# Kernel tuning notes

Hardware: AMD Instinct MI355X
Metric: run time of the kernel (lower is better)

The kernel has to match this reference:

```python
import jax, jax.numpy as jnp
import numpy as np

# dims
B, N, D = 4, 1024, 768
H, HD = 12, 64            # num_heads, head_dim (routed q heads = top-H experts)
EA = 24                   # num_attn_experts
EF, KF = 8, 2             # num_ffd_experts, ffd_heads (top-k for FFN MoE)
HS = int(4 * D) // KF     # ffn expert head_size = 1536
T = 9                     # task_num
S = 1                     # shared FFN experts: max(1, int(8*0.1))


def layernorm(x, g, b, eps=1e-5):
    m = x.mean(-1, keepdims=True)
    v = ((x - m) ** 2).mean(-1, keepdims=True)
    return (x - m) * jax.lax.rsqrt(v + eps) * g + b


def setup_inputs() -> dict:
    key = jax.random.key(0)
    ks = jax.random.split(key, 16)
    s = 0.02
    rn = lambda k, shp: jax.random.normal(k, shp, dtype=jnp.float32)
    return {
        "x": rn(ks[0], (B, N, D)),
        "task_bh": 3,
        "ln1_g": jnp.ones((D,), jnp.float32), "ln1_b": jnp.zeros((D,), jnp.float32),
        "ln2_g": jnp.ones((D,), jnp.float32), "ln2_b": jnp.zeros((D,), jnp.float32),
        "gate_a": rn(ks[1], (T, D, EA)) * s,
        "Wq_in": rn(ks[2], (EA, D, HD)) * s,
        "Wq_out": rn(ks[3], (EA, HD, D)) * s,
        "W_kv": rn(ks[4], (D, 2 * HD)) * s, "b_kv": jnp.zeros((2 * HD,), jnp.float32),
        "gate_f": rn(ks[5], (T, D, EF)) * s,
        "W1f": rn(ks[6], (EF, D, HS)) * s, "b1f": jnp.zeros((EF, HS), jnp.float32),
        "W2f": rn(ks[7], (EF, HS, D)) * s, "b_out": jnp.zeros((D,), jnp.float32),
        "Ws1": rn(ks[8], (S, D, HS)) * s, "bs1": jnp.zeros((S, HS), jnp.float32),
        "Ws2": rn(ks[9], (S, HS, D)) * s,
    }


def _route(h, gate_w, k):
    # h: [B,N,D], gate_w: [D,E] -> normalized top-k weights + one-hot dispatch
    probs = jax.nn.softmax(jnp.einsum("bnd,de->bne", h, gate_w), axis=-1)
    topv, topi = jax.lax.top_k(probs, k)                 # [B,N,k]
    topv = topv / topv.sum(-1, keepdims=True)
    oh = jax.nn.one_hot(topi, probs.shape[-1], dtype=h.dtype)  # [B,N,k,E]
    return topv, oh


def reference(x, task_bh, ln1_g, ln1_b, ln2_g, ln2_b, gate_a, Wq_in, Wq_out,
              W_kv, b_kv, gate_f, W1f, b1f, W2f, b_out, Ws1, bs1, Ws2):
    # --- MoE attention (routed q heads, shared single-head k/v) ---
    h = layernorm(x, ln1_g, ln1_b)
    topv, oh = _route(h, gate_a[task_bh], H)             # [B,N,H], [B,N,H,EA]
    h_all = jnp.einsum("bnd,edh->bneh", h, Wq_in)        # all-expert q projections
    q = jnp.einsum("bnke,bneh->bnkh", oh, h_all)         # gathered q heads [B,N,H,HD]
    kv = h @ W_kv + b_kv
    kk, vv = kv[..., :HD], kv[..., HD:]                  # [B,N,HD]
    att = jnp.einsum("bihd,bjd->bhij", q, kk) * (HD ** -0.5)
    att = jax.nn.softmax(att, axis=-1)
    o = jnp.einsum("bhij,bjd->bihd", att, vv)            # [B,N,H,HD]
    dense = jnp.einsum("bnk,bnke,bnkh->bneh", topv, oh, o)  # scatter to experts
    y = jnp.einsum("bneh,ehd->bnd", dense, Wq_out)       # gated expert output proj
    x = x + y

    # --- MoE FFN (top-KF routed experts + shared experts) ---
    h = layernorm(x, ln2_g, ln2_b)
    topv, oh = _route(h, gate_f[task_bh], KF)            # [B,N,KF], [B,N,KF,EF]
    h_all = jax.nn.gelu(jnp.einsum("bnd,edh->bneh", h, W1f) + b1f, approximate=False)
    wdense = jnp.einsum("bnk,bnke->bne", topv, oh)       # per-expert gate weights
    y = jnp.einsum("bne,bneh,ehd->bnd", wdense, h_all, W2f) + b_out
    hs = jax.nn.gelu(jnp.einsum("bnd,sdh->bnsh", h, Ws1) + bs1, approximate=False)
    y = y + jnp.einsum("bnsh,shd->bnd", hs, Ws2)         # always-on shared experts
    return x + y
```

## Files before the change

### kernel.cpp

```cpp
#include <hip/hip_runtime.h>
#include <hip/hip_bf16.h>

#define NTOK 4096
#define DDIM 768
#define NEA  24
#define NHEAD 12
#define HDIM 64
#define NEF  8
#define HSD  1536
#define SEQL 1024
#define NB   4
#define MAXTILE 104

using bf16 = __hip_bfloat16;

typedef float v4f __attribute__((ext_vector_type(4)));
typedef short v8s __attribute__((ext_vector_type(8)));
typedef __bf16 v8bf __attribute__((ext_vector_type(8)));

typedef __attribute__((address_space(3))) unsigned lds_u32_t;
typedef const __attribute__((address_space(1))) unsigned glb_u32_t;

__device__ __forceinline__ void gload16(const void* g, void* l) {
  __builtin_amdgcn_global_load_lds((glb_u32_t*)g, (lds_u32_t*)l, 16, 0, 0);
}

__device__ __forceinline__ float gelu_f(float x) {
  return 0.5f * x * (1.0f + erff(x * 0.70710678118654752440f));
}

__device__ __forceinline__ short f2bf_s(float x) {
  bf16 h = __float2bfloat16(x);
  return __builtin_bit_cast(short, h);
}

__device__ __forceinline__ void gemm_core(const short* gA0, const short* gA1,
                                          const short* gB0, const short* gB1,
                                          short* lA, short* lB, int steps,
                                          v4f (&acc)[4][4])
{
  const int tid = threadIdx.x;
  const int w = tid >> 6, l = tid & 63;
  const int wr = (w >> 1) * 64, wc = (w & 1) * 64;
  const int fr = l & 15, ko = (l >> 4) * 8;
  const int sb = w * 1024;
  gload16(gA0, lA + sb); gload16(gA1, lA + sb + 512);
  gload16(gB0, lB + sb); gload16(gB1, lB + sb + 512);
  gA0 += 32; gA1 += 32; gB0 += 32; gB1 += 32;
  __syncthreads();
  int cur = 0;
  for (int s = 0; s < steps; ++s) {
    const int nxt = cur ^ 1;
    if (s + 1 < steps) {
      gload16(gA0, lA + nxt * 4096 + sb);
      gload16(gA1, lA + nxt * 4096 + sb + 512);
      gload16(gB0, lB + nxt * 4096 + sb);
      gload16(gB1, lB + nxt * 4096 + sb + 512);
      gA0 += 32; gA1 += 32; gB0 += 32; gB1 += 32;
    }
    const short* bA = lA + cur * 4096;
    const short* bB = lB + cur * 4096;
    v8s av[4], bv[4];
#pragma unroll
    for (int mi = 0; mi < 4; ++mi)
      av[mi] = *(const v8s*)(bA + (wr + mi * 16 + fr) * 32 + ko);
#pragma unroll
    for (int ni = 0; ni < 4; ++ni)
      bv[ni] = *(const v8s*)(bB + (wc + ni * 16 + fr) * 32 + ko);
#pragma unroll
    for (int mi = 0; mi < 4; ++mi)
#pragma unroll
      for (int ni = 0; ni < 4; ++ni)
        acc[mi][ni] = __builtin_amdgcn_mfma_f32_16x16x32_bf16(
            __builtin_bit_cast(v8bf, av[mi]), __builtin_bit_cast(v8bf, bv[ni]),
            acc[mi][ni], 0, 0, 0);
    __syncthreads();
    cur = nxt;
  }
}

template<int EPI>
__global__ __launch_bounds__(256, 4) void k_gemm(const short* __restrict__ A,
    const short* __restrict__ Bt, float* __restrict__ C,
    const float* __restrict__ bias, const float* __restrict__ addsrc,
    int N, int K)
{
  __shared__ __align__(16) short lA[2 * 128 * 32];
  __shared__ __align__(16) short lB[2 * 128 * 32];
  const int tid = threadIdx.x, w = tid >> 6, l = tid & 63;
  const int m0 = blockIdx.x * 128, n0 = blockIdx.y * 128;
  const int ca = w * 128 + l, cb = ca + 64;
  const short* gA0 = A + (size_t)(m0 + (ca >> 2)) * K + (ca & 3) * 8;
  const short* gA1 = A + (size_t)(m0 + (cb >> 2)) * K + (cb & 3) * 8;
  const short* gB0 = Bt + (size_t)(n0 + (ca >> 2)) * K + (ca & 3) * 8;
  const short* gB1 = Bt + (size_t)(n0 + (cb >> 2)) * K + (cb & 3) * 8;
  v4f acc[4][4];
  v4f z = {0.f, 0.f, 0.f, 0.f};
#pragma unroll
  for (int i = 0; i < 4; ++i)
#pragma unroll
    for (int j = 0; j < 4; ++j) acc[i][j] = z;
  gemm_core(gA0, gA1, gB0, gB1, lA, lB, K >> 5, acc);
  const int wr = (w >> 1) * 64, wc = (w & 1) * 64;
  const int fr = l & 15, rq = (l >> 4) * 4;
#pragma unroll
  for (int mi = 0; mi < 4; ++mi)
#pragma unroll
    for (int ni = 0; ni < 4; ++ni)
#pragma unroll
      for (int j = 0; j < 4; ++j) {
        int rg = m0 + wr + mi * 16 + rq + j;
        int cg = n0 + wc + ni * 16 + fr;
        float v = acc[mi][ni][j];
        if (EPI == 1) v += bias[cg];
        if (EPI == 2) v += addsrc[(size_t)rg * N + cg];
        C[(size_t)rg * N + cg] = v;
      }
}

template<int PHASE>
__global__ __launch_bounds__(256, 4) void k_gemm_moe(
    const short* __restrict__ Aact, const short* __restrict__ Wt,
    const short* __restrict__ Wst, const float* __restrict__ b1f,
    const float* __restrict__ bs1, const float* __restrict__ wsl,
    const int* __restrict__ off, const int* __restrict__ cnt,
    const int* __restrict__ list, const int* __restrict__ tmeta,
    const int* __restrict__ ntl, short* __restrict__ outb,
    float* __restrict__ outf)
{
  constexpr int K = (PHASE == 0) ? DDIM : HSD;
  constexpr int N = (PHASE == 0) ? HSD : DDIM;
  const int ti = blockIdx.x;
  if (ti >= ntl[0]) return;
  const int mm = tmeta[ti];
  const int e = mm >> 20;
  const int r0 = mm & 0xFFFFF;
  const int base = (e < 8) ? off[e] : NTOK * 2;
  const int c    = (e < 8) ? cnt[e] : NTOK;
  const int rows = c - r0;
  const short* Bt = (e < 8) ? Wt + (size_t)e * N * K : Wst;
  __shared__ __align__(16) short lA[2 * 128 * 32];
  __shared__ __align__(16) short lB[2 * 128 * 32];
  const int tid = threadIdx.x, w = tid >> 6, l = tid & 63;
  const int n0 = blockIdx.y * 128;
  const int ca = w * 128 + l, cb = ca + 64;

  auto arowptr = [&](int chunk) -> const short* {
    int r = chunk >> 2;
    int re = (r < rows) ? r : (rows - 1);
    int slot = base + r0 + re;
    if (PHASE == 0) {
      int tok = (e < 8) ? list[slot] : (slot - NTOK * 2);
      return Aact + (size_t)tok * DDIM;
    } else {
      return Aact + (size_t)slot * HSD;
    }
  };
  const short* gA0 = arowptr(ca) + (ca & 3) * 8;
  const short* gA1 = arowptr(cb) + (cb & 3) * 8;
  const short* gB0 = Bt + (size_t)(n0 + (ca >> 2)) * K + (ca & 3) * 8;
  const short* gB1 = Bt + (size_t)(n0 + (cb >> 2)) * K + (cb & 3) * 8;
  v4f acc[4][4];
  v4f z = {0.f, 0.f, 0.f, 0.f};
#pragma unroll
  for (int i = 0; i < 4; ++i)
#pragma unroll
    for (int j = 0; j < 4; ++j) acc[i][j] = z;
  gemm_core(gA0, gA1, gB0, gB1, lA, lB, K >> 5, acc);
  const int wr = (w >> 1) * 64, wc = (w & 1) * 64;
  const int fr = l & 15, rq = (l >> 4) * 4;
  const float* bias = (PHASE == 0) ? ((e < 8) ? b1f + e * HSD : bs1) : nullptr;
#pragma unroll
  for (int mi = 0; mi < 4; ++mi)
#pragma unroll
    for (int ni = 0; ni < 4; ++ni)
#pragma unroll
      for (int j = 0; j < 4; ++j) {
        int rl = wr + mi * 16 + rq + j;
        if (rl >= rows) continue;
        int slot = base + r0 + rl;
        int cg = n0 + wc + ni * 16 + fr;
        float v = acc[mi][ni][j];
        if (PHASE == 0) {
          v = gelu_f(v + bias[cg]);
          outb[(size_t)slot * HSD + cg] = f2bf_s(v);
        } else {
          outf[(size_t)slot * DDIM + cg] = v * wsl[slot];
        }
      }
}

__global__ __launch_bounds__(256) void k_ln(const float* __restrict__ x,
    const float* __restrict__ g, const float* __restrict__ b,
    float* __restrict__ hf, bf16* __restrict__ hb)
{
  const size_t t = blockIdx.x;
  const float* xr = x + t * DDIM;
  int tid = threadIdx.x;
  float v0 = xr[tid], v1 = xr[tid + 256], v2 = xr[tid + 512];
  float s = v0 + v1 + v2;
  float q = v0 * v0 + v1 * v1 + v2 * v2;
  for (int m = 32; m >= 1; m >>= 1) { s += __shfl_xor(s, m); q += __shfl_xor(q, m); }
  __shared__ float rs[4], rq[4];
  int w = tid >> 6, l = tid & 63;
  if (l == 0) { rs[w] = s; rq[w] = q; }
  __syncthreads();
  s = rs[0] + rs[1] + rs[2] + rs[3];
  q = rq[0] + rq[1] + rq[2] + rq[3];
  float mean = s * (1.f / DDIM);
  float var = q * (1.f / DDIM) - mean * mean;
  float inv = rsqrtf(var + 1e-5f);
  float vv[3] = {v0, v1, v2};
#pragma unroll
  for (int i = 0; i < 3; ++i) {
    int d = tid + i * 256;
    float y = (vv[i] - mean) * inv * g[d] + b[d];
    hf[t * DDIM + d] = y;
    hb[t * DDIM + d] = __float2bfloat16(y);
  }
}

__global__ __launch_bounds__(256) void k_routeA(const float* __restrict__ hf,
    const float* __restrict__ gt, int* __restrict__ topi, float* __restrict__ topv)
{
  const int t = blockIdx.x * 4 + (threadIdx.x >> 6);
  const int l = threadIdx.x & 63;
  const float* h = hf + (size_t)t * DDIM;
  float hr[12];
#pragma unroll
  for (int m = 0; m < 12; ++m) hr[m] = h[l + 64 * m];
  float lg[NEA];
#pragma unroll
  for (int e = 0; e < NEA; ++e) {
    const float* ge = gt + e * DDIM;
    float a = 0.f;
#pragma unroll
    for (int m = 0; m < 12; ++m) a += hr[m] * ge[l + 64 * m];
#pragma unroll
    for (int m = 32; m >= 1; m >>= 1) a += __shfl_xor(a, m);
    lg[e] = a;
  }
  unsigned used = 0;
  int sel[NHEAD]; float bvk[NHEAD];
#pragma unroll
  for (int k = 0; k < NHEAD; ++k) {
    float bv = -3e30f; int best = 0;
#pragma unroll
    for (int e = 0; e < NEA; ++e)
      if (!((used >> e) & 1u) && lg[e] > bv) { bv = lg[e]; best = e; }
    used |= 1u << best; sel[k] = best; bvk[k] = bv;
  }
  const float mx = bvk[0];
  float pvk[NHEAD], ssum = 0.f;
#pragma unroll
  for (int k = 0; k < NHEAD; ++k) { pvk[k] = expf(bvk[k] - mx); ssum += pvk[k]; }
  const float inv = 1.f / ssum;
  if (l == 0) {
#pragma unroll
    for (int k = 0; k < NHEAD; ++k) {
      topi[t * NHEAD + k] = sel[k];
      topv[t * NHEAD + k] = pvk[k] * inv;
    }
  }
}

__global__ __launch_bounds__(256) void k_routeF(const float* __restrict__ hf,
    const float* __restrict__ gt, int* __restrict__ ef, float* __restrict__ wf,
    int* __restrict__ cnt)
{
  const int t = blockIdx.x * 4 + (threadIdx.x >> 6);
  const int l = threadIdx.x & 63;
  const float* h = hf + (size_t)t * DDIM;
  float hr[12];
#pragma unroll
  for (int m = 0; m < 12; ++m) hr[m] = h[l + 64 * m];
  float lg[NEF];
#pragma unroll
  for (int e = 0; e < NEF; ++e) {
    const float* ge = gt + e * DDIM;
    float a = 0.f;
#pragma unroll
    for (int m = 0; m < 12; ++m) a += hr[m] * ge[l + 64 * m];
#pragma unroll
    for (int m = 32; m >= 1; m >>= 1) a += __shfl_xor(a, m);
    lg[e] = a;
  }
  unsigned used = 0;
  int sel[2]; float bvk[2];
#pragma unroll
  for (int k = 0; k < 2; ++k) {
    float bv = -3e30f; int best = 0;
#pragma unroll
    for (int e = 0; e < NEF; ++e)
      if (!((used >> e) & 1u) && lg[e] > bv) { bv = lg[e]; best = e; }
    used |= 1u << best; sel[k] = best; bvk[k] = bv;
  }
  const float mx = bvk[0];
  float p0 = expf(bvk[0] - mx), p1 = expf(bvk[1] - mx);
  const float inv = 1.f / (p0 + p1);
  if (l == 0) {
    ef[t * 2 + 0] = sel[0]; wf[t * 2 + 0] = p0 * inv;
    ef[t * 2 + 1] = sel[1]; wf[t * 2 + 1] = p1 * inv;
    atomicAdd(&cnt[sel[0]], 1);
    atomicAdd(&cnt[sel[1]], 1);
  }
}

__global__ void k_packGT(const float* __restrict__ src, const int* __restrict__ task,
                         float* __restrict__ dst, int E)
{
  int idx = blockIdx.x * 256 + threadIdx.x;
  if (idx >= E * DDIM) return;
  int e = idx / DDIM, d = idx - e * DDIM;
  dst[idx] = src[(size_t)task[0] * DDIM * E + (size_t)d * E + e];
}

__global__ void k_off(const int* __restrict__ cnt, int* __restrict__ off,
                      int* __restrict__ cur, int* __restrict__ tmeta,
                      int* __restrict__ ntl)
{
  if (threadIdx.x == 0 && blockIdx.x == 0) {
    int a = 0;
    for (int e = 0; e < NEF; ++e) { off[e] = a; cur[e] = a; a += cnt[e]; }
    off[NEF] = a;
    int n = 0;
    for (int e = 0; e < NEF; ++e)
      for (int r = 0; r < cnt[e]; r += 128) tmeta[n++] = (e << 20) | r;
    for (int r = 0; r < NTOK; r += 128) tmeta[n++] = (8 << 20) | r;
    ntl[0] = n;
  }
}

__global__ void k_fill(const int* __restrict__ ef, const float* __restrict__ wf,
                       int* __restrict__ cur, int* __restrict__ list,
                       float* __restrict__ wsl, int* __restrict__ sof)
{
  int t = blockIdx.x * 256 + threadIdx.x;
  if (t >= NTOK) return;
  for (int k = 0; k < 2; ++k) {
    int e = ef[t * 2 + k];
    int slot = atomicAdd(&cur[e], 1);
    list[slot] = t;
    wsl[slot] = wf[t * 2 + k];
    sof[t * 2 + k] = slot;
  }
  list[NTOK * 2 + t] = t;
  wsl[NTOK * 2 + t] = 1.f;
}

__global__ void k_qgather(const float* __restrict__ hallq, const int* __restrict__ topi,
                          bf16* __restrict__ q)
{
  int idx = blockIdx.x * 256 + threadIdx.x;
  int t = idx / (NHEAD * HDIM);
  int rem = idx - t * (NHEAD * HDIM);
  int k = rem >> 6, hd = rem & 63;
  q[idx] = __float2bfloat16(
      hallq[(size_t)t * (NEA * HDIM) + topi[t * NHEAD + k] * HDIM + hd]);
}

__global__ void k_packKV(const float* __restrict__ kvf, bf16* __restrict__ kvb)
{
  int i = blockIdx.x * 256 + threadIdx.x;
  float4 v = *(const float4*)&kvf[(size_t)i * 4];
  kvb[(size_t)i * 4 + 0] = __float2bfloat16(v.x);
  kvb[(size_t)i * 4 + 1] = __float2bfloat16(v.y);
  kvb[(size_t)i * 4 + 2] = __float2bfloat16(v.z);
  kvb[(size_t)i * 4 + 3] = __float2bfloat16(v.w);
}

__global__ void k_scatter(const float* __restrict__ o, const int* __restrict__ topi,
                          const float* __restrict__ topv, bf16* __restrict__ dense)
{
  int idx = blockIdx.x * 256 + threadIdx.x;
  int t = idx / (NHEAD * HDIM);
  int rem = idx - t * (NHEAD * HDIM);
  int k = rem >> 6, hd = rem & 63;
  float v = topv[t * NHEAD + k] * o[idx];
  dense[(size_t)t * (NEA * HDIM) + topi[t * NHEAD + k] * HDIM + hd] = __float2bfloat16(v);
}

__global__ __launch_bounds__(256, 2) void k_attn_mfma(const bf16* __restrict__ q,
    const bf16* __restrict__ kv, float* __restrict__ o)
{
  __shared__ __align__(16) short Qs[64 * 64];
  __shared__ __align__(16) short Ks[64 * 64];
  __shared__ __align__(16) short Vs[64 * 64];
  __shared__ __align__(16) short Ps[64 * 64];
  const int i0 = blockIdx.x * 64;
  const int h = blockIdx.y;
  const int b = blockIdx.z;
  const int tid = threadIdx.x;
  const int w = tid >> 6, l = tid & 63;
  const int g = l >> 4, fq = l & 15;
  const short* qg = (const short*)q;
  const short* kvg = (const short*)kv;

  {
    int c0 = tid, c1 = tid + 256;
    int r0 = c0 >> 3, s0 = (c0 & 7) ^ (r0 & 7);
    int r1 = c1 >> 3, s1 = (c1 & 7) ^ (r1 & 7);
    gload16(qg + ((size_t)((b * SEQL + i0 + r0) * NHEAD + h)) * HDIM + s0 * 8,
            Qs + w * 512);
    gload16(qg + ((size_t)((b * SEQL + i0 + r1) * NHEAD + h)) * HDIM + s1 * 8,
            Qs + 2048 + w * 512);
  }

  float m_run[4], l_run[4];
  v4f oacc[4];
#pragma unroll
  for (int r = 0; r < 4; ++r) { m_run[r] = -1e30f; l_run[r] = 0.f; }
#pragma unroll
  for (int nd = 0; nd < 4; ++nd) oacc[nd] = (v4f){0.f, 0.f, 0.f, 0.f};

  const int vj = tid & 63;
  const int vd0 = (tid >> 6) * 16;

  for (int jt = 0; jt < 16; ++jt) {
    if (jt) __syncthreads();
    {
      int c0 = tid, c1 = tid + 256;
      int r0 = c0 >> 3, s0 = (c0 & 7) ^ (r0 & 7);
      int r1 = c1 >> 3, s1 = (c1 & 7) ^ (r1 & 7);
      gload16(kvg + ((size_t)(b * SEQL + jt * 64 + r0)) * 128 + s0 * 8,
              Ks + w * 512);
      gload16(kvg + ((size_t)(b * SEQL + jt * 64 + r1)) * 128 + s1 * 8,
              Ks + 2048 + w * 512);
    }
    {
      const short* gv = kvg + ((size_t)(b * SEQL + jt * 64 + vj)) * 128 + 64 + vd0;
      v8s a0 = *(const v8s*)gv;
      v8s a1 = *(const v8s*)(gv + 8);
#pragma unroll
      for (int k2 = 0; k2 < 8; ++k2) {
        int d = vd0 + k2;
        Vs[d * 64 + (((vj >> 3) ^ (d & 7)) << 3) + (vj & 7)] = a0[k2];
      }
#pragma unroll
      for (int k2 = 0; k2 < 8; ++k2) {
        int d = vd0 + 8 + k2;
        Vs[d * 64 + (((vj >> 3) ^ (d & 7)) << 3) + (vj & 7)] = a1[k2];
      }
    }
    __syncthreads();

    v8s aq[2];
#pragma unroll
    for (int kk = 0; kk < 2; ++kk)
      aq[kk] = *(const v8s*)&Qs[(16 * w + fq) * 64 + (((kk * 4 + g) ^ (fq & 7)) << 3)];
    v4f sacc[4];
#pragma unroll
    for (int n = 0; n < 4; ++n) {
      sacc[n] = (v4f){0.f, 0.f, 0.f, 0.f};
#pragma unroll
      for (int kk = 0; kk < 2; ++kk) {
        v8s bk = *(const v8s*)&Ks[(16 * n + fq) * 64 + (((kk * 4 + g) ^ (fq & 7)) << 3)];
        sacc[n] = __builtin_amdgcn_mfma_f32_16x16x32_bf16(
            __builtin_bit_cast(v8bf, aq[kk]), __builtin_bit_cast(v8bf, bk),
            sacc[n], 0, 0, 0);
      }
    }
#pragma unroll
    for (int n = 0; n < 4; ++n) sacc[n] *= 0.125f;

#pragma unroll
    for (int r = 0; r < 4; ++r) {
      float mt = fmaxf(fmaxf(sacc[0][r], sacc[1][r]), fmaxf(sacc[2][r], sacc[3][r]));
      mt = fmaxf(mt, __shfl_xor(mt, 1));
      mt = fmaxf(mt, __shfl_xor(mt, 2));
      mt = fmaxf(mt, __shfl_xor(mt, 4));
      mt = fmaxf(mt, __shfl_xor(mt, 8));
      float mnew = fmaxf(m_run[r], mt);
      float corr = __expf(m_run[r] - mnew);
      float pv[4], ps = 0.f;
#pragma unroll
      for (int n = 0; n < 4; ++n) { pv[n] = __expf(sacc[n][r] - mnew); ps += pv[n]; }
      ps += __shfl_xor(ps, 1);
      ps += __shfl_xor(ps, 2);
      ps += __shfl_xor(ps, 4);
      ps += __shfl_xor(ps, 8);
      l_run[r] = l_run[r] * corr + ps;
      m_run[r] = mnew;
#pragma unroll
      for (int nd = 0; nd < 4; ++nd) oacc[nd][r] *= corr;
      int qrow = 16 * w + 4 * g + r;
#pragma unroll
      for (int n = 0; n < 4; ++n)
        Ps[qrow * 64 + (((2 * n + (fq >> 3)) ^ (qrow & 7)) << 3) + (fq & 7)] =
            f2bf_s(pv[n]);
    }
    asm volatile("s_waitcnt lgkmcnt(0)" ::: "memory");
    __builtin_amdgcn_sched_barrier(0);

#pragma unroll
    for (int kk = 0; kk < 2; ++kk) {
      v8s pa = *(const v8s*)&Ps[(16 * w + fq) * 64 + (((kk * 4 + g) ^ (fq & 7)) << 3)];
#pragma unroll
      for (int nd = 0; nd < 4; ++nd) {
        v8s vb = *(const v8s*)&Vs[(16 * nd + fq) * 64 + (((kk * 4 + g) ^ (fq & 7)) << 3)];
        oacc[nd] = __builtin_amdgcn_mfma_f32_16x16x32_bf16(
            __builtin_bit_cast(v8bf, pa), __builtin_bit_cast(v8bf, vb),
            oacc[nd], 0, 0, 0);
      }
    }
  }

#pragma unroll
  for (int r = 0; r < 4; ++r) {
    float inv = 1.f / l_run[r];
    int qgl = i0 + 16 * w + 4 * g + r;
#pragma unroll
    for (int nd = 0; nd < 4; ++nd)
      o[(((size_t)b * SEQL + qgl) * NHEAD + h) * HDIM + 16 * nd + fq] =
          oacc[nd][r] * inv;
  }
}

__global__ __launch_bounds__(256) void k_packT(const float* __restrict__ src,
                                               bf16* __restrict__ dst, int K, int N)
{
  __shared__ float tile[32][33];
  const size_t zoff = (size_t)blockIdx.z * K * N;
  const int k0 = blockIdx.x * 32, n0 = blockIdx.y * 32;
  const int tx = threadIdx.x & 31, ty = threadIdx.x >> 5;
#pragma unroll
  for (int i = 0; i < 32; i += 8)
    tile[ty + i][tx] = src[zoff + (size_t)(k0 + ty + i) * N + n0 + tx];
  __syncthreads();
#pragma unroll
  for (int i = 0; i < 32; i += 8)
    dst[zoff + (size_t)(n0 + ty + i) * K + k0 + tx] =
        __float2bfloat16(tile[tx][ty + i]);
}

__global__ void k_final(const float* __restrict__ x2, const float* __restrict__ bout,
                        const float* __restrict__ yp, const int* __restrict__ sof,
                        float* __restrict__ out)
{
  int idx = blockIdx.x * 256 + threadIdx.x;
  int t = idx / DDIM, d = idx - t * DDIM;
  int s0 = sof[2 * t], s1 = sof[2 * t + 1];
  out[idx] = x2[idx] + bout[d] + yp[(size_t)s0 * DDIM + d] + yp[(size_t)s1 * DDIM + d] +
             yp[((size_t)(NTOK * 2) + t) * DDIM + d];
}

extern "C" void kernel_launch(void* const* d_in, const int* in_sizes, int n_in,
                              void* d_out, int out_size, void* d_ws, size_t ws_size,
                              hipStream_t stream) {
  const float* x      = (const float*)d_in[0];
  const int*   task   = (const int*)d_in[1];
  const float* ln1g   = (const float*)d_in[2];
  const float* ln1b   = (const float*)d_in[3];
  const float* ln2g   = (const float*)d_in[4];
  const float* ln2b   = (const float*)d_in[5];
  const float* gate_a = (const float*)d_in[6];
  const float* wq_in  = (const float*)d_in[7];
  const float* wq_out = (const float*)d_in[8];
  const float* w_kv   = (const float*)d_in[9];
  const float* b_kv   = (const float*)d_in[10];
  const float* gate_f = (const float*)d_in[11];
  const float* w1f    = (const float*)d_in[12];
  const float* b1f    = (const float*)d_in[13];
  const float* w2f    = (const float*)d_in[14];
  const float* b_out  = (const float*)d_in[15];
  const float* ws1    = (const float*)d_in[16];
  const float* bs1    = (const float*)d_in[17];
  const float* ws2    = (const float*)d_in[18];

  char* W = (char*)d_ws;
  size_t off_ = 0;
  auto alloc = [&](size_t b) { size_t o = off_; off_ += (b + 255) & ~(size_t)255; return o; };
  size_t o_h1f   = alloc(12582912);
  size_t o_h1b   = alloc(6291456);
  size_t o_hallq = alloc(25165824);
  size_t o_hmid  = o_h1f;
  size_t o_q     = alloc(12582912);
  size_t o_o     = alloc(12582912);
  size_t o_dense = alloc(12582912);
  size_t o_ypart = o_q;
  size_t o_kv    = alloc(2097152);
  size_t o_kvb   = alloc(1048576);
  size_t o_x2    = alloc(12582912);
  size_t o_h2f   = alloc(12582912);
  size_t o_h2b   = alloc(6291456);
  size_t o_btq   = alloc(2359296);
  size_t o_wkvt  = alloc(196608);
  size_t o_wqot  = alloc(2359296);
  size_t o_w1t   = alloc(18874368);
  size_t o_w2t   = alloc(18874368);
  size_t o_ws1t  = alloc(2359296);
  size_t o_ws2t  = alloc(2359296);
  size_t o_topi  = alloc(196608);
  size_t o_topv  = alloc(196608);
  size_t o_ef    = alloc(32768);
  size_t o_wf    = alloc(32768);
  size_t o_cnt   = alloc(1024);
  size_t o_offs  = alloc(1024);
  size_t o_cur   = alloc(1024);
  size_t o_list  = alloc(49152);
  size_t o_wsl   = alloc(49152);
  size_t o_sof   = alloc(32768);
  size_t o_tmeta = alloc(1024);
  size_t o_ntl   = alloc(256);
  size_t o_gta   = alloc(73728);
  size_t o_gtf   = alloc(24576);
  if (ws_size < off_) return;

  float* h1f   = (float*)(W + o_h1f);
  bf16*  h1b   = (bf16*)(W + o_h1b);
  float* hallq = (float*)(W + o_hallq);
  bf16*  qbb   = (bf16*)(W + o_q);
  float* ob    = (float*)(W + o_o);
  bf16*  dense = (bf16*)(W + o_dense);
  float* kvb   = (float*)(W + o_kv);
  bf16*  kvbb  = (bf16*)(W + o_kvb);
  float* x2b   = (float*)(W + o_x2);
  float* h2f   = (float*)(W + o_h2f);
  bf16*  h2b   = (bf16*)(W + o_h2b);
  short* hmid  = (short*)(W + o_hmid);
  float* ypart = (float*)(W + o_ypart);
  int*   topi  = (int*)(W + o_topi);
  float* topv  = (float*)(W + o_topv);
  int*   efp   = (int*)(W + o_ef);
  float* wfp   = (float*)(W + o_wf);
  int*   cntp  = (int*)(W + o_cnt);
  int*   offp  = (int*)(W + o_offs);
  int*   curp  = (int*)(W + o_cur);
  int*   listp = (int*)(W + o_list);
  float* wslp  = (float*)(W + o_wsl);
  int*   sofp  = (int*)(W + o_sof);
  int*   tmeta = (int*)(W + o_tmeta);
  int*   ntl   = (int*)(W + o_ntl);
  float* gta   = (float*)(W + o_gta);
  float* gtf   = (float*)(W + o_gtf);

  k_packT<<<dim3(24, 2, 24), 256, 0, stream>>>(wq_in, (bf16*)(W + o_btq), 768, 64);
  k_packT<<<dim3(24, 4, 1), 256, 0, stream>>>(w_kv, (bf16*)(W + o_wkvt), 768, 128);
  k_packT<<<dim3(48, 24, 1), 256, 0, stream>>>(wq_out, (bf16*)(W + o_wqot), 1536, 768);
  k_packT<<<dim3(24, 48, 8), 256, 0, stream>>>(w1f, (bf16*)(W + o_w1t), 768, 1536);
  k_packT<<<dim3(48, 24, 8), 256, 0, stream>>>(w2f, (bf16*)(W + o_w2t), 1536, 768);
  k_packT<<<dim3(24, 48, 1), 256, 0, stream>>>(ws1, (bf16*)(W + o_ws1t), 768, 1536);
  k_packT<<<dim3(48, 24, 1), 256, 0, stream>>>(ws2, (bf16*)(W + o_ws2t), 1536, 768);
  k_packGT<<<dim3(72), 256, 0, stream>>>(gate_a, task, gta, NEA);
  k_packGT<<<dim3(24), 256, 0, stream>>>(gate_f, task, gtf, NEF);

  (void)hipMemsetAsync(W + o_dense, 0, 12582912, stream);
  (void)hipMemsetAsync(W + o_cnt, 0, 64, stream);

  k_ln<<<NTOK, 256, 0, stream>>>(x, ln1g, ln1b, h1f, h1b);
  k_routeA<<<NTOK / 4, 256, 0, stream>>>(h1f, gta, topi, topv);

  k_gemm<0><<<dim3(32, 12), 256, 0, stream>>>((const short*)h1b, (const short*)(W + o_btq),
                                              hallq, nullptr, nullptr, 1536, 768);
  k_gemm<1><<<dim3(32, 1), 256, 0, stream>>>((const short*)h1b, (const short*)(W + o_wkvt),
                                             kvb, b_kv, nullptr, 128, 768);

  k_qgather<<<dim3(12288), 256, 0, stream>>>(hallq, topi, qbb);
  k_packKV<<<dim3(512), 256, 0, stream>>>(kvb, kvbb);
  k_attn_mfma<<<dim3(16, NHEAD, NB), 256, 0, stream>>>(qbb, kvbb, ob);
  k_scatter<<<dim3(12288), 256, 0, stream>>>(ob, topi, topv, dense);

  k_gemm<2><<<dim3(32, 6), 256, 0, stream>>>((const short*)dense, (const short*)(W + o_wqot),
                                             x2b, nullptr, x, 768, 1536);

  k_ln<<<NTOK, 256, 0, stream>>>(x2b, ln2g, ln2b, h2f, h2b);
  k_routeF<<<NTOK / 4, 256, 0, stream>>>(h2f, gtf, efp, wfp, cntp);
  k_off<<<1, 1, 0, stream>>>(cntp, offp, curp, tmeta, ntl);
  k_fill<<<16, 256, 0, stream>>>(efp, wfp, curp, listp, wslp, sofp);

  k_gemm_moe<0><<<dim3(MAXTILE, 12), 256, 0, stream>>>((const short*)h2b,
      (const short*)(W + o_w1t), (const short*)(W + o_ws1t), b1f, bs1, nullptr,
      offp, cntp, listp, tmeta, ntl, hmid, nullptr);
  k_gemm_moe<1><<<dim3(MAXTILE, 6), 256, 0, stream>>>((const short*)hmid,
      (const short*)(W + o_w2t), (const short*)(W + o_ws2t), nullptr, nullptr, wslp,
      offp, cntp, listp, tmeta, ntl, nullptr, ypart);

  k_final<<<dim3(12288), 256, 0, stream>>>(x2b, b_out, ypart, sofp, (float*)d_out);
}
```

Baseline: 551.0 us.

## Triple-buffer GEMM LDS staging with explicit vmcnt waits and raw barriers

Moves the shared GEMM core from double to triple buffering. Loads now run two K-steps ahead, and each step waits only with s_waitcnt vmcnt(4) instead of a full __syncthreads drain, so global-to-LDS loads can overlap more MFMA work. This raises LDS per block from 32KB to 48KB, which may limit how many blocks fit per CU. It also depends on the raw barrier plus waitcnt being correct for direct-to-LDS loads.

```diff
diff --git a/kernel.cpp b/kernel.cpp
--- a/kernel.cpp
+++ b/kernel.cpp
@@ -44,19 +44,28 @@
   const int wr = (w >> 1) * 64, wc = (w & 1) * 64;
   const int fr = l & 15, ko = (l >> 4) * 8;
   const int sb = w * 1024;
-  gload16(gA0, lA + sb); gload16(gA1, lA + sb + 512);
-  gload16(gB0, lB + sb); gload16(gB1, lB + sb + 512);
-  gA0 += 32; gA1 += 32; gB0 += 32; gB1 += 32;
-  __syncthreads();
+  auto stage = [&](int buf) {
+    gload16(gA0, lA + buf * 4096 + sb);
+    gload16(gA1, lA + buf * 4096 + sb + 512);
+    gload16(gB0, lB + buf * 4096 + sb);
+    gload16(gB1, lB + buf * 4096 + sb + 512);
+    gA0 += 32; gA1 += 32; gB0 += 32; gB1 += 32;
+  };
+  stage(0);
+  if (steps > 1) {
+    stage(1);
+    asm volatile("s_waitcnt vmcnt(4)" ::: "memory");
+  } else {
+    asm volatile("s_waitcnt vmcnt(0)" ::: "memory");
+  }
+  __builtin_amdgcn_s_barrier();
+  __builtin_amdgcn_sched_barrier(0);
+
   int cur = 0;
   for (int s = 0; s < steps; ++s) {
-    const int nxt = cur ^ 1;
-    if (s + 1 < steps) {
-      gload16(gA0, lA + nxt * 4096 + sb);
-      gload16(gA1, lA + nxt * 4096 + sb + 512);
-      gload16(gB0, lB + nxt * 4096 + sb);
-      gload16(gB1, lB + nxt * 4096 + sb + 512);
-      gA0 += 32; gA1 += 32; gB0 += 32; gB1 += 32;
+    if (s + 2 < steps) {
+      int nb = cur + 2; if (nb >= 3) nb -= 3;
+      stage(nb);
     }
     const short* bA = lA + cur * 4096;
     const short* bB = lB + cur * 4096;
@@ -74,8 +83,16 @@
         acc[mi][ni] = __builtin_amdgcn_mfma_f32_16x16x32_bf16(
             __builtin_bit_cast(v8bf, av[mi]), __builtin_bit_cast(v8bf, bv[ni]),
             acc[mi][ni], 0, 0, 0);
-    __syncthreads();
-    cur = nxt;
+    if (s + 2 < steps) {
+      asm volatile("s_waitcnt vmcnt(4)" ::: "memory");
+    } else if (s + 1 < steps) {
+      asm volatile("s_waitcnt vmcnt(0)" ::: "memory");
+    }
+    if (s + 1 < steps) {
+      __builtin_amdgcn_s_barrier();
+      __builtin_amdgcn_sched_barrier(0);
+    }
+    ++cur; if (cur >= 3) cur -= 3;
   }
 }
 
@@ -85,8 +102,8 @@
     const float* __restrict__ bias, const float* __restrict__ addsrc,
     int N, int K)
 {
-  __shared__ __align__(16) short lA[2 * 128 * 32];
-  __shared__ __align__(16) short lB[2 * 128 * 32];
+  __shared__ __align__(16) short lA[3 * 128 * 32];
+  __shared__ __align__(16) short lB[3 * 128 * 32];
   const int tid = threadIdx.x, w = tid >> 6, l = tid & 63;
   const int m0 = blockIdx.x * 128, n0 = blockIdx.y * 128;
   const int ca = w * 128 + l, cb = ca + 64;
@@ -139,8 +156,8 @@
   const int c    = (e < 8) ? cnt[e] : NTOK;
   const int rows = c - r0;
   const short* Bt = (e < 8) ? Wt + (size_t)e * N * K : Wst;
-  __shared__ __align__(16) short lA[2 * 128 * 32];
-  __shared__ __align__(16) short lB[2 * 128 * 32];
+  __shared__ __align__(16) short lA[3 * 128 * 32];
+  __shared__ __align__(16) short lB[3 * 128 * 32];
   const int tid = threadIdx.x, w = tid >> 6, l = tid & 63;
   const int n0 = blockIdx.y * 128;
   const int ca = w * 128 + l, cb = ca + 64;
```

Result: slower. 576.2 us (+4.6%).

## Enlarge MoE FFN GEMM tiles to 256x256 with split-K atomics for down projection

Applied to the files above, without the earlier changes.

Replaces the 128x128 MoE expert GEMM with a 512-thread 256x256 tile kernel that has its own double-buffered MFMA loop, and regroups the tile metadata in 256-row chunks. The down projection is split over K into two halves, each accumulated into the output with float atomicAdd, and the output buffer is zeroed with a memset first. The goal is more operand reuse per block and fewer weight reloads. In exchange, partially filled expert tiles waste more work, there are fewer blocks to spread across the GPU, and the atomics plus the memset add traffic.

```diff
diff --git a/kernel.cpp b/kernel.cpp
--- a/kernel.cpp
+++ b/kernel.cpp
@@ -10,7 +10,7 @@
 #define HSD  1536
 #define SEQL 1024
 #define NB   4
-#define MAXTILE 104
+#define MAXT256 64
 
 using bf16 = __hip_bfloat16;
 
@@ -119,7 +119,7 @@
 }
 
 template<int PHASE>
-__global__ __launch_bounds__(256, 4) void k_gemm_moe(
+__global__ __launch_bounds__(512, 2) void k_moe256(
     const short* __restrict__ Aact, const short* __restrict__ Wt,
     const short* __restrict__ Wst, const float* __restrict__ b1f,
     const float* __restrict__ bs1, const float* __restrict__ wsl,
@@ -139,53 +139,87 @@
   const int c    = (e < 8) ? cnt[e] : NTOK;
   const int rows = c - r0;
   const short* Bt = (e < 8) ? Wt + (size_t)e * N * K : Wst;
-  __shared__ __align__(16) short lA[2 * 128 * 32];
-  __shared__ __align__(16) short lB[2 * 128 * 32];
+  const int kbase = (PHASE == 1) ? (int)blockIdx.z * 768 : 0;
+  __shared__ __align__(16) short lA[2 * 256 * 32];
+  __shared__ __align__(16) short lB[2 * 256 * 32];
   const int tid = threadIdx.x, w = tid >> 6, l = tid & 63;
-  const int n0 = blockIdx.y * 128;
-  const int ca = w * 128 + l, cb = ca + 64;
-
-  auto arowptr = [&](int chunk) -> const short* {
-    int r = chunk >> 2;
+  const int n0 = blockIdx.y * 256;
+
+  auto arow = [&](int r) -> const short* {
     int re = (r < rows) ? r : (rows - 1);
     int slot = base + r0 + re;
     if (PHASE == 0) {
       int tok = (e < 8) ? list[slot] : (slot - NTOK * 2);
       return Aact + (size_t)tok * DDIM;
-    } else {
-      return Aact + (size_t)slot * HSD;
     }
+    return Aact + (size_t)slot * HSD;
   };
-  const short* gA0 = arowptr(ca) + (ca & 3) * 8;
-  const short* gA1 = arowptr(cb) + (cb & 3) * 8;
-  const short* gB0 = Bt + (size_t)(n0 + (ca >> 2)) * K + (ca & 3) * 8;
-  const short* gB1 = Bt + (size_t)(n0 + (cb >> 2)) * K + (cb & 3) * 8;
-  v4f acc[4][4];
+  const short* gA0 = arow(tid >> 2) + (tid & 3) * 8 + kbase;
+  const short* gA1 = arow((tid >> 2) + 128) + (tid & 3) * 8 + kbase;
+  const short* gB0 = Bt + (size_t)(n0 + (tid >> 2)) * K + (tid & 3) * 8 + kbase;
+  const short* gB1 = gB0 + (size_t)128 * K;
+  const int wm = w >> 2, wn = w & 3;
+  const int fr = l & 15, ko = (l >> 4) * 8;
+
+  v4f acc[8][4];
   v4f z = {0.f, 0.f, 0.f, 0.f};
 #pragma unroll
-  for (int i = 0; i < 4; ++i)
+  for (int i = 0; i < 8; ++i)
 #pragma unroll
     for (int j = 0; j < 4; ++j) acc[i][j] = z;
-  gemm_core(gA0, gA1, gB0, gB1, lA, lB, K >> 5, acc);
-  const int wr = (w >> 1) * 64, wc = (w & 1) * 64;
-  const int fr = l & 15, rq = (l >> 4) * 4;
+
+  auto stage = [&](int buf) {
+    gload16(gA0, lA + buf * 8192 + w * 512);
+    gload16(gA1, lA + buf * 8192 + 4096 + w * 512);
+    gload16(gB0, lB + buf * 8192 + w * 512);
+    gload16(gB1, lB + buf * 8192 + 4096 + w * 512);
+    gA0 += 32; gA1 += 32; gB0 += 32; gB1 += 32;
+  };
+  const int steps = 768 >> 5;
+  stage(0);
+  __syncthreads();
+  int cur = 0;
+  for (int s = 0; s < steps; ++s) {
+    const int nxt = cur ^ 1;
+    if (s + 1 < steps) stage(nxt);
+    const short* bA = lA + cur * 8192;
+    const short* bB = lB + cur * 8192;
+    v8s av[8], bv[4];
+#pragma unroll
+    for (int mi = 0; mi < 8; ++mi)
+      av[mi] = *(const v8s*)(bA + (wm * 128 + mi * 16 + fr) * 32 + ko);
+#pragma unroll
+    for (int ni = 0; ni < 4; ++ni)
+      bv[ni] = *(const v8s*)(bB + (wn * 64 + ni * 16 + fr) * 32 + ko);
+#pragma unroll
+    for (int mi = 0; mi < 8; ++mi)
+#pragma unroll
+      for (int ni = 0; ni < 4; ++ni)
+        acc[mi][ni] = __builtin_amdgcn_mfma_f32_16x16x32_bf16(
+            __builtin_bit_cast(v8bf, av[mi]), __builtin_bit_cast(v8bf, bv[ni]),
+            acc[mi][ni], 0, 0, 0);
+    __syncthreads();
+    cur = nxt;
+  }
+
+  const int rq = (l >> 4) * 4;
   const float* bias = (PHASE == 0) ? ((e < 8) ? b1f + e * HSD : bs1) : nullptr;
 #pragma unroll
-  for (int mi = 0; mi < 4; ++mi)
+  for (int mi = 0; mi < 8; ++mi)
 #pragma unroll
     for (int ni = 0; ni < 4; ++ni)
 #pragma unroll
       for (int j = 0; j < 4; ++j) {
-        int rl = wr + mi * 16 + rq + j;
+        int rl = wm * 128 + mi * 16 + rq + j;
         if (rl >= rows) continue;
         int slot = base + r0 + rl;
-        int cg = n0 + wc + ni * 16 + fr;
+        int cg = n0 + wn * 64 + ni * 16 + fr;
         float v = acc[mi][ni][j];
         if (PHASE == 0) {
           v = gelu_f(v + bias[cg]);
           outb[(size_t)slot * HSD + cg] = f2bf_s(v);
         } else {
-          outf[(size_t)slot * DDIM + cg] = v * wsl[slot];
+          atomicAdd(&outf[(size_t)slot * DDIM + cg], v * wsl[slot]);
         }
       }
 }
@@ -325,8 +359,8 @@
     off[NEF] = a;
     int n = 0;
     for (int e = 0; e < NEF; ++e)
-      for (int r = 0; r < cnt[e]; r += 128) tmeta[n++] = (e << 20) | r;
-    for (int r = 0; r < NTOK; r += 128) tmeta[n++] = (8 << 20) | r;
+      for (int r = 0; r < cnt[e]; r += 256) tmeta[n++] = (e << 20) | r;
+    for (int r = 0; r < NTOK; r += 256) tmeta[n++] = (8 << 20) | r;
     ntl[0] = n;
   }
 }
@@ -663,15 +697,17 @@
   k_gemm<2><<<dim3(32, 6), 256, 0, stream>>>((const short*)dense, (const short*)(W + o_wqot),
                                              x2b, nullptr, x, 768, 1536);
 
+  (void)hipMemsetAsync(W + o_ypart, 0, 37748736, stream);
+
   k_ln<<<NTOK, 256, 0, stream>>>(x2b, ln2g, ln2b, h2f, h2b);
   k_routeF<<<NTOK / 4, 256, 0, stream>>>(h2f, gtf, efp, wfp, cntp);
   k_off<<<1, 1, 0, stream>>>(cntp, offp, curp, tmeta, ntl);
   k_fill<<<16, 256, 0, stream>>>(efp, wfp, curp, listp, wslp, sofp);
 
-  k_gemm_moe<0><<<dim3(MAXTILE, 12), 256, 0, stream>>>((const short*)h2b,
+  k_moe256<0><<<dim3(MAXT256, 6), 512, 0, stream>>>((const short*)h2b,
       (const short*)(W + o_w1t), (const short*)(W + o_ws1t), b1f, bs1, nullptr,
       offp, cntp, listp, tmeta, ntl, hmid, nullptr);
-  k_gemm_moe<1><<<dim3(MAXTILE, 6), 256, 0, stream>>>((const short*)hmid,
+  k_moe256<1><<<dim3(MAXT256, 3, 2), 512, 0, stream>>>((const short*)hmid,
       (const short*)(W + o_w2t), (const short*)(W + o_ws2t), nullptr, nullptr, wslp,
       offp, cntp, listp, tmeta, ntl, nullptr, ypart);
 
```

After: 756.3 us. 1.37x slower.

## Fuse KV projection into Q GEMM, add XCD swizzle, raise MoE occupancy

Applied to the files above, without the earlier changes.

Appends the packed W_kv columns to the all-expert Q weight matrix so a single GEMM with N=1664 produces both q projections and k/v, removing a separate underfilled 32-block GEMM launch. The kv bias is now added in packKV, which reads straight from the combined output. Both GEMM kernels remap block indices with an XCD-aware swizzle so that neighbouring tiles land on the same chiplet for L2 reuse. MoE GEMM launch bounds are raised to 5 waves per SIMD, which may force register spilling.

```diff
diff --git a/kernel.cpp b/kernel.cpp
--- a/kernel.cpp
+++ b/kernel.cpp
@@ -11,6 +11,7 @@
 #define SEQL 1024
 #define NB   4
 #define MAXTILE 104
+#define NQKV 1664
 
 using bf16 = __hip_bfloat16;
 
@@ -32,6 +33,10 @@
 __device__ __forceinline__ short f2bf_s(float x) {
   bf16 h = __float2bfloat16(x);
   return __builtin_bit_cast(short, h);
+}
+
+__device__ __forceinline__ int xcd_swz(int lin, int nwg) {
+  return (lin & 7) * (nwg >> 3) + (lin >> 3);
 }
 
 __device__ __forceinline__ void gemm_core(const short* gA0, const short* gA1,
@@ -82,13 +87,14 @@
 template<int EPI>
 __global__ __launch_bounds__(256, 4) void k_gemm(const short* __restrict__ A,
     const short* __restrict__ Bt, float* __restrict__ C,
-    const float* __restrict__ bias, const float* __restrict__ addsrc,
-    int N, int K)
-{
+    const float* __restrict__ addsrc, int N, int K)
+{
+  const int nwg = gridDim.x * gridDim.y;
+  const int swz = xcd_swz(blockIdx.x + gridDim.x * blockIdx.y, nwg);
+  const int m0 = (swz % gridDim.x) * 128, n0 = (swz / gridDim.x) * 128;
   __shared__ __align__(16) short lA[2 * 128 * 32];
   __shared__ __align__(16) short lB[2 * 128 * 32];
   const int tid = threadIdx.x, w = tid >> 6, l = tid & 63;
-  const int m0 = blockIdx.x * 128, n0 = blockIdx.y * 128;
   const int ca = w * 128 + l, cb = ca + 64;
   const short* gA0 = A + (size_t)(m0 + (ca >> 2)) * K + (ca & 3) * 8;
   const short* gA1 = A + (size_t)(m0 + (cb >> 2)) * K + (cb & 3) * 8;
@@ -112,14 +118,13 @@
         int rg = m0 + wr + mi * 16 + rq + j;
         int cg = n0 + wc + ni * 16 + fr;
         float v = acc[mi][ni][j];
-        if (EPI == 1) v += bias[cg];
         if (EPI == 2) v += addsrc[(size_t)rg * N + cg];
         C[(size_t)rg * N + cg] = v;
       }
 }
 
 template<int PHASE>
-__global__ __launch_bounds__(256, 4) void k_gemm_moe(
+__global__ __launch_bounds__(256, 5) void k_gemm_moe(
     const short* __restrict__ Aact, const short* __restrict__ Wt,
     const short* __restrict__ Wst, const float* __restrict__ b1f,
     const float* __restrict__ bs1, const float* __restrict__ wsl,
@@ -130,7 +135,10 @@
 {
   constexpr int K = (PHASE == 0) ? DDIM : HSD;
   constexpr int N = (PHASE == 0) ? HSD : DDIM;
-  const int ti = blockIdx.x;
+  const int nwg = gridDim.x * gridDim.y;
+  const int swz = xcd_swz(blockIdx.x + gridDim.x * blockIdx.y, nwg);
+  const int ti = swz % gridDim.x;
+  const int n0 = (swz / gridDim.x) * 128;
   if (ti >= ntl[0]) return;
   const int mm = tmeta[ti];
   const int e = mm >> 20;
@@ -142,7 +150,6 @@
   __shared__ __align__(16) short lA[2 * 128 * 32];
   __shared__ __align__(16) short lB[2 * 128 * 32];
   const int tid = threadIdx.x, w = tid >> 6, l = tid & 63;
-  const int n0 = blockIdx.y * 128;
   const int ca = w * 128 + l, cb = ca + 64;
 
   auto arowptr = [&](int chunk) -> const short* {
@@ -356,17 +363,15 @@
   int rem = idx - t * (NHEAD * HDIM);
   int k = rem >> 6, hd = rem & 63;
   q[idx] = __float2bfloat16(
-      hallq[(size_t)t * (NEA * HDIM) + topi[t * NHEAD + k] * HDIM + hd]);
-}
-
-__global__ void k_packKV(const float* __restrict__ kvf, bf16* __restrict__ kvb)
-{
-  int i = blockIdx.x * 256 + threadIdx.x;
-  float4 v = *(const float4*)&kvf[(size_t)i * 4];
-  kvb[(size_t)i * 4 + 0] = __float2bfloat16(v.x);
-  kvb[(size_t)i * 4 + 1] = __float2bfloat16(v.y);
-  kvb[(size_t)i * 4 + 2] = __float2bfloat16(v.z);
-  kvb[(size_t)i * 4 + 3] = __float2bfloat16(v.w);
+      hallq[(size_t)t * NQKV + topi[t * NHEAD + k] * HDIM + hd]);
+}
+
+__global__ void k_packKV(const float* __restrict__ hallq, const float* __restrict__ bkv,
+                         bf16* __restrict__ kvb)
+{
+  int idx = blockIdx.x * 256 + threadIdx.x;
+  int t = idx >> 7, j = idx & 127;
+  kvb[idx] = __float2bfloat16(hallq[(size_t)t * NQKV + 1536 + j] + bkv[j]);
 }
 
 __global__ void k_scatter(const float* __restrict__ o, const int* __restrict__ topi,
@@ -572,19 +577,17 @@
   auto alloc = [&](size_t b) { size_t o = off_; off_ += (b + 255) & ~(size_t)255; return o; };
   size_t o_h1f   = alloc(12582912);
   size_t o_h1b   = alloc(6291456);
-  size_t o_hallq = alloc(25165824);
+  size_t o_hallq = alloc(27262976);
   size_t o_hmid  = o_h1f;
   size_t o_q     = alloc(12582912);
   size_t o_o     = alloc(12582912);
   size_t o_dense = alloc(12582912);
   size_t o_ypart = o_q;
-  size_t o_kv    = alloc(2097152);
   size_t o_kvb   = alloc(1048576);
   size_t o_x2    = alloc(12582912);
   size_t o_h2f   = alloc(12582912);
   size_t o_h2b   = alloc(6291456);
-  size_t o_btq   = alloc(2359296);
-  size_t o_wkvt  = alloc(196608);
+  size_t o_btq   = alloc(2555904);
   size_t o_wqot  = alloc(2359296);
   size_t o_w1t   = alloc(18874368);
   size_t o_w2t   = alloc(18874368);
@@ -612,7 +615,6 @@
   bf16*  qbb   = (bf16*)(W + o_q);
   float* ob    = (float*)(W + o_o);
   bf16*  dense = (bf16*)(W + o_dense);
-  float* kvb   = (float*)(W + o_kv);
   bf16*  kvbb  = (bf16*)(W + o_kvb);
   float* x2b   = (float*)(W + o_x2);
   float* h2f   = (float*)(W + o_h2f);
@@ -635,7 +637,7 @@
   float* gtf   = (float*)(W + o_gtf);
 
   k_packT<<<dim3(24, 2, 24), 256, 0, stream>>>(wq_in, (bf16*)(W + o_btq), 768, 64);
-  k_packT<<<dim3(24, 4, 1), 256, 0, stream>>>(w_kv, (bf16*)(W + o_wkvt), 768, 128);
+  k_packT<<<dim3(24, 4, 1), 256, 0, stream>>>(w_kv, (bf16*)(W + o_btq) + 1536 * 768, 768, 128);
   k_packT<<<dim3(48, 24, 1), 256, 0, stream>>>(wq_out, (bf16*)(W + o_wqot), 1536, 768);
   k_packT<<<dim3(24, 48, 8), 256, 0, stream>>>(w1f, (bf16*)(W + o_w1t), 768, 1536);
   k_packT<<<dim3(48, 24, 8), 256, 0, stream>>>(w2f, (bf16*)(W + o_w2t), 1536, 768);
@@ -650,18 +652,16 @@
   k_ln<<<NTOK, 256, 0, stream>>>(x, ln1g, ln1b, h1f, h1b);
   k_routeA<<<NTOK / 4, 256, 0, stream>>>(h1f, gta, topi, topv);
 
-  k_gemm<0><<<dim3(32, 12), 256, 0, stream>>>((const short*)h1b, (const short*)(W + o_btq),
-                                              hallq, nullptr, nullptr, 1536, 768);
-  k_gemm<1><<<dim3(32, 1), 256, 0, stream>>>((const short*)h1b, (const short*)(W + o_wkvt),
-                                             kvb, b_kv, nullptr, 128, 768);
+  k_gemm<0><<<dim3(32, 13), 256, 0, stream>>>((const short*)h1b, (const short*)(W + o_btq),
+                                              hallq, nullptr, NQKV, 768);
 
   k_qgather<<<dim3(12288), 256, 0, stream>>>(hallq, topi, qbb);
-  k_packKV<<<dim3(512), 256, 0, stream>>>(kvb, kvbb);
+  k_packKV<<<dim3(2048), 256, 0, stream>>>(hallq, b_kv, kvbb);
   k_attn_mfma<<<dim3(16, NHEAD, NB), 256, 0, stream>>>(qbb, kvbb, ob);
   k_scatter<<<dim3(12288), 256, 0, stream>>>(ob, topi, topv, dense);
 
   k_gemm<2><<<dim3(32, 6), 256, 0, stream>>>((const short*)dense, (const short*)(W + o_wqot),
-                                             x2b, nullptr, x, 768, 1536);
+                                             x2b, x, 768, 1536);
 
   k_ln<<<NTOK, 256, 0, stream>>>(x2b, ln2g, ln2b, h2f, h2b);
   k_routeF<<<NTOK / 4, 256, 0, stream>>>(h2f, gtf, efp, wfp, cntp);
```

After: 558.7 us. Within noise of the previous version (+1.4%).
